# Kernel tuning notes

Measured on AMD Instinct MI355X. Metric: run time of the kernel, lower is better.

## Reference

```python
import jax, jax.numpy as jnp
import numpy as np

N = 100_000      # nodes
E = 1_600_000    # edges (avg degree 16)
D_IN, D_PROJ, D_HID = 128, 128, 64


def setup_inputs() -> dict:
    key = jax.random.key(0)
    ks = jax.random.split(key, 10)
    glorot = lambda k, i, o: jax.random.normal(k, (i, o), jnp.float32) * jnp.sqrt(2.0 / (i + o))
    x = jax.random.normal(ks[0], (N, D_IN), jnp.float32)
    edge_index = jax.random.randint(ks[1], (2, E), 0, N, dtype=jnp.int32)
    # encoder: GCN(input->proj), ReLU, GCN(proj->hidden)
    W1, b1 = glorot(ks[2], D_IN, D_PROJ), jnp.zeros((D_PROJ,), jnp.float32)
    W2, b2 = glorot(ks[3], D_PROJ, D_HID), jnp.zeros((D_HID,), jnp.float32)
    # contra_head: GCN(hidden->proj), ReLU, GCN(proj->input)
    W3, b3 = glorot(ks[4], D_HID, D_PROJ), jnp.zeros((D_PROJ,), jnp.float32)
    W4, b4 = glorot(ks[5], D_PROJ, D_IN), jnp.zeros((D_IN,), jnp.float32)
    return dict(x=x, W1=W1, b1=b1, W2=W2, b2=b2, W3=W3, b3=b3, W4=W4, b4=b4,
                edge_index=edge_index)


def gcn_layer(x, W, b, src, dst, deg, inv_sqrt_deg):
    """PyG GCNConv: out = D^{-1/2}(A+I)D^{-1/2} (x W) + b, unit edge weights."""
    h = x @ W                                   # [N, out]
    norm = inv_sqrt_deg[src] * inv_sqrt_deg[dst]  # [E]
    agg = jax.ops.segment_sum(h[src] * norm[:, None], dst, num_segments=x.shape[0])
    agg = agg + h * (1.0 / deg)[:, None]        # self-loop term: 1/deg_i
    return agg + b


def reference(x, W1, b1, W2, b2, W3, b3, W4, b4, edge_index):
    src, dst = edge_index[0], edge_index[1]
    # gcn_norm degrees (with self-loop, unit weights) — shared across layers
    deg = jax.ops.segment_sum(jnp.ones(src.shape[0], x.dtype), dst,
                              num_segments=x.shape[0]) + 1.0
    isd = jax.lax.rsqrt(deg)
    # encoder
    z = gcn_layer(x, W1, b1, src, dst, deg, isd)
    z = jax.nn.relu(z)
    z = gcn_layer(z, W2, b2, src, dst, deg, isd)
    # contra_head
    z = gcn_layer(z, W3, b3, src, dst, deg, isd)
    z = jax.nn.relu(z)
    z = gcn_layer(z, W4, b4, src, dst, deg, isd)
    return z
```

## Files before the change

### kernel.cpp

```cpp
#include <hip/hip_runtime.h>
#include <hip/hip_fp16.h>

typedef _Float16 f16x8 __attribute__((ext_vector_type(8)));
typedef float f32x4 __attribute__((ext_vector_type(4)));

#define CHUNK 2048
#define BSHIFT 9
#define CAP 12288


static __global__ void binpass_kernel(const int* __restrict__ src, const int* __restrict__ dst,
                                      int* __restrict__ bucket_cur, int2* __restrict__ pairs,
                                      int E, int NB) {
  __shared__ int lh[256], lbase[256], lcur[256];
  int t = threadIdx.x;
  lh[t] = 0;
  __syncthreads();
  int base = blockIdx.x * CHUNK;
  int end = min(base + CHUNK, E);
  for (int i = base + t; i < end; i += 256)
    atomicAdd(&lh[dst[i] >> BSHIFT], 1);
  __syncthreads();
  if (t < NB && lh[t]) lbase[t] = atomicAdd(&bucket_cur[t], lh[t]);
  lcur[t] = 0;
  __syncthreads();
  for (int i = base + t; i < end; i += 256) {
    int s = src[i], d = dst[i];
    int b = d >> BSHIFT;
    int p = lbase[b] + atomicAdd(&lcur[b], 1);
    if (p < CAP) pairs[(size_t)b * CAP + p] = make_int2(s, d);
  }
}

static __global__ void bedge_scan_kernel(const int* __restrict__ bucket_cur,
                                         int* __restrict__ bucket_base,
                                         int* __restrict__ row_ptr, int NB, int n, int E) {
  __shared__ int sh[256];
  int t = threadIdx.x;
  int v = (t < NB) ? bucket_cur[t] : 0;
  sh[t] = v;
  __syncthreads();
  for (int off = 1; off < 256; off <<= 1) {
    int x = (t >= off) ? sh[t - off] : 0;
    __syncthreads();
    sh[t] += x;
    __syncthreads();
  }
  if (t < NB) bucket_base[t] = sh[t] - v;
  if (t == 0) row_ptr[n] = E;
}

static __global__ void bucket_work_kernel(const int2* __restrict__ pairs,
                                          const int* __restrict__ bucket_cur,
                                          const int* __restrict__ bucket_base,
                                          float* __restrict__ isd, int* __restrict__ row_ptr,
                                          int* __restrict__ csr_src, int n) {
  __shared__ int lcnt[512];
  __shared__ int lcur[512];
  __shared__ int s2[256];
  int b = blockIdx.x;
  int t = threadIdx.x;
  int d0 = b << BSHIFT;
  int cnt = bucket_cur[b];
  int base = bucket_base[b];
  const int2* bp = pairs + (size_t)b * CAP;
  lcnt[t] = 0;
  lcnt[t + 256] = 0;
  __syncthreads();
  for (int i = t; i < cnt; i += 256)
    atomicAdd(&lcnt[bp[i].y - d0], 1);
  __syncthreads();
  int a0 = lcnt[2 * t], a1 = lcnt[2 * t + 1];
  s2[t] = a0 + a1;
  __syncthreads();
  for (int off = 1; off < 256; off <<= 1) {
    int x = (t >= off) ? s2[t - off] : 0;
    __syncthreads();
    s2[t] += x;
    __syncthreads();
  }
  int excl = s2[t] - (a0 + a1);
  int d = d0 + 2 * t;
  if (d < n)     { row_ptr[d]     = base + excl;      isd[d]     = rsqrtf((float)a0 + 1.0f); }
  if (d + 1 < n) { row_ptr[d + 1] = base + excl + a0; isd[d + 1] = rsqrtf((float)a1 + 1.0f); }
  lcur[2 * t] = excl;
  lcur[2 * t + 1] = excl + a0;
  __syncthreads();
  for (int i = t; i < cnt; i += 256) {
    int2 e = bp[i];
    int p = atomicAdd(&lcur[e.y - d0], 1);
    csr_src[base + p] = e.x;
  }
}

template<int K, int NOUT, bool AHALF, int EPI>
__device__ __forceinline__ void gemm_mfma_body(const void* __restrict__ Xin,
                                               const float* __restrict__ W,
                                               const float* __restrict__ aux,
                                               __half* __restrict__ H, int n) {
  __shared__ _Float16 ah[64][K + 8];
  __shared__ _Float16 bh[64][K + 8];
  const int tid = threadIdx.x;
  const int bm = blockIdx.x * 64;
  const int bc = blockIdx.y * 64;

  if (AHALF) {
    const __half* Xh = (const __half*)Xin;
    for (int i = tid; i < 64 * (K / 8); i += 256) {
      int r = i / (K / 8), c8 = i % (K / 8);
      int gr = bm + r;
      f16x8 v = {};
      if (gr < n) v = *(const f16x8*)&Xh[(size_t)gr * K + c8 * 8];
      *(f16x8*)&ah[r][c8 * 8] = v;
    }
  } else {
    const float* Xf = (const float*)Xin;
    for (int i = tid; i < 64 * (K / 8); i += 256) {
      int r = i / (K / 8), c8 = i % (K / 8);
      int gr = bm + r;
      f16x8 v = {};
      if (gr < n) {
        float4 a = *(const float4*)&Xf[(size_t)gr * K + c8 * 8];
        float4 b = *(const float4*)&Xf[(size_t)gr * K + c8 * 8 + 4];
        v[0] = (_Float16)a.x; v[1] = (_Float16)a.y; v[2] = (_Float16)a.z; v[3] = (_Float16)a.w;
        v[4] = (_Float16)b.x; v[5] = (_Float16)b.y; v[6] = (_Float16)b.z; v[7] = (_Float16)b.w;
      }
      *(f16x8*)&ah[r][c8 * 8] = v;
    }
  }
  {
    const int nn = tid & 63;
    const int kq = tid >> 6;
    constexpr int KT = K / 4;
#pragma unroll
    for (int k8 = 0; k8 < KT; k8 += 8) {
      int k0 = kq * KT + k8;
      f16x8 v;
#pragma unroll
      for (int j = 0; j < 8; ++j)
        v[j] = (_Float16)W[(size_t)(k0 + j) * NOUT + bc + nn];
      *(f16x8*)&bh[nn][k0] = v;
    }
  }
  __syncthreads();

  const int lane = tid & 63;
  const int wid = tid >> 6;
  const int wm = (wid >> 1) * 32;
  const int wn = (wid & 1) * 32;
  const int lr = lane & 15;
  const int lk = (lane >> 4) * 8;

  f32x4 acc[2][2] = {};
#pragma unroll
  for (int ks = 0; ks < K; ks += 32) {
    f16x8 a0 = *(const f16x8*)&ah[wm + lr][ks + lk];
    f16x8 a1 = *(const f16x8*)&ah[wm + 16 + lr][ks + lk];
    f16x8 b0 = *(const f16x8*)&bh[wn + lr][ks + lk];
    f16x8 b1 = *(const f16x8*)&bh[wn + 16 + lr][ks + lk];
    acc[0][0] = __builtin_amdgcn_mfma_f32_16x16x32_f16(a0, b0, acc[0][0], 0, 0, 0);
    acc[0][1] = __builtin_amdgcn_mfma_f32_16x16x32_f16(a0, b1, acc[0][1], 0, 0, 0);
    acc[1][0] = __builtin_amdgcn_mfma_f32_16x16x32_f16(a1, b0, acc[1][0], 0, 0, 0);
    acc[1][1] = __builtin_amdgcn_mfma_f32_16x16x32_f16(a1, b1, acc[1][1], 0, 0, 0);
  }

  float bcol0 = 0.f, bcol1 = 0.f;
  if (EPI == 1) {
    bcol0 = aux[bc + wn + lr];
    bcol1 = aux[bc + wn + 16 + lr];
  }
  const int rgrp = (lane >> 4) * 4;
#pragma unroll
  for (int tm = 0; tm < 2; ++tm) {
    int rb = bm + wm + tm * 16 + rgrp;
#pragma unroll
    for (int r = 0; r < 4; ++r) {
      int row = rb + r;
      if (row >= n) continue;
      float s = (EPI == 0) ? aux[row] : 0.f;
#pragma unroll
      for (int tn = 0; tn < 2; ++tn) {
        int col = bc + wn + tn * 16 + lr;
        float v = acc[tm][tn][r];
        if (EPI == 0) v *= s;
        else v = fmaxf(v + (tn ? bcol1 : bcol0), 0.f);
        H[(size_t)row * NOUT + col] = __float2half(v);
      }
    }
  }
}

#define DEF_GEMM(NAME, K, NOUT, AHALF, EPI)                                              \
  __global__ __launch_bounds__(256, 2) void NAME(const void* __restrict__ X,             \
                                                 const float* __restrict__ W,            \
                                                 const float* __restrict__ aux,          \
                                                 __half* __restrict__ H, int n) {        \
    gemm_mfma_body<K, NOUT, AHALF, EPI>(X, W, aux, H, n);                                \
  }
DEF_GEMM(gemm1_mfma_k128_n128, 128, 128, false, 0)
DEF_GEMM(gemm2_mfma_k128_n64, 128, 64, true, 0)
DEF_GEMM(gemm3_mfma_k64_n128, 64, 128, true, 1)
DEF_GEMM(gemm4_mfma_k128_n128, 128, 128, true, 0)

template<int D, bool RELU, bool HASBIAS, bool POSTSCALE, bool OUTHALF>
__device__ __forceinline__ void agg_body(const __half* __restrict__ hs, const int* __restrict__ row_ptr,
                                         const int* __restrict__ csr_src, const float* __restrict__ isd,
                                         const float* __restrict__ bias, void* __restrict__ out, int n) {
  int gt = blockIdx.x * blockDim.x + threadIdx.x;
  int gw, l;
  if (D == 128) {
    gw = gt >> 6;
    l = threadIdx.x & 63;
  } else {
    gw = (gt >> 6) * 2 + ((threadIdx.x >> 5) & 1);
    l = threadIdx.x & 31;
  }
  if (gw >= n) return;

  float wd = isd[gw];
  float2 hv = __half22float2(*(const __half2*)(hs + (size_t)gw * D + l * 2));
  float2 bv = make_float2(0.f, 0.f);
  if (HASBIAS) bv = *(const float2*)(bias + l * 2);

  int beg = row_ptr[gw], end = row_ptr[gw + 1];
  float acc0 = 0.f, acc1 = 0.f;

  int e = beg;
  int s0 = 0, s1 = 0, s2 = 0, s3 = 0;
  if (e + 4 <= end) {
    s0 = csr_src[e + 0]; s1 = csr_src[e + 1];
    s2 = csr_src[e + 2]; s3 = csr_src[e + 3];
  }
  while (e + 4 <= end) {
    float2 v0 = __half22float2(*(const __half2*)(hs + (size_t)s0 * D + l * 2));
    float2 v1 = __half22float2(*(const __half2*)(hs + (size_t)s1 * D + l * 2));
    float2 v2 = __half22float2(*(const __half2*)(hs + (size_t)s2 * D + l * 2));
    float2 v3 = __half22float2(*(const __half2*)(hs + (size_t)s3 * D + l * 2));
    int en = e + 4;
    if (en + 4 <= end) {
      s0 = csr_src[en + 0]; s1 = csr_src[en + 1];
      s2 = csr_src[en + 2]; s3 = csr_src[en + 3];
    }
    acc0 += (v0.x + v1.x) + (v2.x + v3.x);
    acc1 += (v0.y + v1.y) + (v2.y + v3.y);
    e = en;
  }
  for (; e < end; ++e) {
    int s = csr_src[e];
    float2 v = __half22float2(*(const __half2*)(hs + (size_t)s * D + l * 2));
    acc0 += v.x;
    acc1 += v.y;
  }

  float o0 = wd * (acc0 + hv.x);
  float o1 = wd * (acc1 + hv.y);
  if (HASBIAS) { o0 += bv.x; o1 += bv.y; }
  if (RELU) { o0 = fmaxf(o0, 0.f); o1 = fmaxf(o1, 0.f); }
  if (POSTSCALE) { o0 *= wd; o1 *= wd; }
  if (OUTHALF) {
    *(__half2*)((__half*)out + (size_t)gw * D + l * 2) = __floats2half2_rn(o0, o1);
  } else {
    *(float2*)((float*)out + (size_t)gw * D + l * 2) = make_float2(o0, o1);
  }
}

#define DEF_AGG(NAME, D, RELU, HASBIAS, POSTSCALE, OUTHALF)                                \
  __global__ void NAME(const __half* __restrict__ hs, const int* __restrict__ row_ptr,     \
                       const int* __restrict__ csr_src, const float* __restrict__ isd,     \
                       const float* __restrict__ bias, void* __restrict__ out, int n) {    \
    agg_body<D, RELU, HASBIAS, POSTSCALE, OUTHALF>(hs, row_ptr, csr_src, isd, bias, out, n); \
  }
DEF_AGG(agg1_d128_biasrelu_f16, 128, true, true, false, true)
DEF_AGG(agg2_d64_bias_ps_f16, 64, false, true, true, true)
DEF_AGG(agg3_d64_plain_f16, 64, false, false, false, true)
DEF_AGG(agg4_d128_bias_f32, 128, false, true, false, false)

static inline size_t align_up(size_t x, size_t a) { return (x + a - 1) & ~(a - 1); }

extern "C" void kernel_launch(void* const* d_in, const int* in_sizes, int n_in,
                              void* d_out, int out_size, void* d_ws, size_t ws_size,
                              hipStream_t stream) {
  const float* X  = (const float*)d_in[0];
  const float* W1 = (const float*)d_in[1];
  const float* b1 = (const float*)d_in[2];
  const float* W2 = (const float*)d_in[3];
  const float* b2 = (const float*)d_in[4];
  const float* W3 = (const float*)d_in[5];
  const float* b3 = (const float*)d_in[6];
  const float* W4 = (const float*)d_in[7];
  const float* b4 = (const float*)d_in[8];
  const int*   ei = (const int*)d_in[9];

  const int N = in_sizes[0] / 128;
  const int E = in_sizes[9] / 2;
  const int* src = ei;
  const int* dst = ei + E;
  float* OUT = (float*)d_out;

  const int NB = (N + (1 << BSHIFT) - 1) >> BSHIFT;
  const int NCH = (E + CHUNK - 1) / CHUNK;

  char* ws = (char*)d_ws;
  size_t off = 0;
  auto alloc = [&](size_t bytes) { void* p = ws + off; off = align_up(off + bytes, 256); return p; };
  int*    row_ptr     = (int*)alloc(((size_t)N + 1) * 4);
  float*  isd         = (float*)alloc((size_t)N * 4);
  int*    csr_src     = (int*)alloc((size_t)E * 4);
  int*    bucket_cur  = (int*)alloc(256 * 4);
  int*    bucket_base = (int*)alloc(256 * 4);
  __half* B1          = (__half*)alloc((size_t)N * 128 * 2);
  __half* B2          = (__half*)alloc((size_t)N * 128 * 2);
  __half* Fa = B1;
  __half* Fb = B1 + (size_t)N * 64;
  int2*   pairs = (int2*)B1;

  hipMemsetAsync(bucket_cur, 0, 256 * 4, stream);

  binpass_kernel<<<NCH, 256, 0, stream>>>(src, dst, bucket_cur, pairs, E, NB);
  bedge_scan_kernel<<<1, 256, 0, stream>>>(bucket_cur, bucket_base, row_ptr, NB, N, E);
  bucket_work_kernel<<<NB, 256, 0, stream>>>(pairs, bucket_cur, bucket_base, isd, row_ptr, csr_src, N);

  const int gm = (N + 63) / 64;
  const int ab128 = (int)(((size_t)N * 64 + 255) / 256);
  const int ab64  = (int)(((size_t)N * 32 + 255) / 256);

  gemm1_mfma_k128_n128<<<dim3(gm, 2), 256, 0, stream>>>(X, W1, isd, B1, N);
  agg1_d128_biasrelu_f16<<<ab128, 256, 0, stream>>>(B1, row_ptr, csr_src, isd, b1, B2, N);
  gemm2_mfma_k128_n64<<<dim3(gm, 1), 256, 0, stream>>>(B2, W2, isd, Fa, N);
  agg2_d64_bias_ps_f16<<<ab64, 256, 0, stream>>>(Fa, row_ptr, csr_src, isd, b2, Fb, N);
  agg3_d64_plain_f16<<<ab64, 256, 0, stream>>>(Fb, row_ptr, csr_src, isd, nullptr, Fa, N);
  gemm3_mfma_k64_n128<<<dim3(gm, 2), 256, 0, stream>>>(Fa, W3, b3, B2, N);
  gemm4_mfma_k128_n128<<<dim3(gm, 2), 256, 0, stream>>>(B2, W4, isd, B1, N);
  agg4_d128_bias_f32<<<ab128, 256, 0, stream>>>(B1, row_ptr, csr_src, isd, b4, OUT, N);
}
```

Baseline: 333.9 us.

## Pre-convert inputs and weights to fp16, widen GEMM tiles, vectorize aggregation lanes

Adds a separate kernel that converts X to fp16 and another that transposes all weights to fp16 once, so the GEMMs load pre-transposed half weights with vector loads. Each GEMM block now computes the full output width instead of splitting columns across two blocks, which avoids reloading the A tile. The aggregation kernels switch to 4 halves per lane, packing more nodes per wavefront. The binning chunk size is also doubled. The X conversion adds an extra pass over the input in exchange for cheaper GEMM loads.

```diff
diff --git a/kernel.cpp b/kernel.cpp
--- a/kernel.cpp
+++ b/kernel.cpp
@@ -2,9 +2,10 @@
 #include <hip/hip_fp16.h>
 
 typedef _Float16 f16x8 __attribute__((ext_vector_type(8)));
+typedef _Float16 f16x4 __attribute__((ext_vector_type(4)));
 typedef float f32x4 __attribute__((ext_vector_type(4)));
 
-#define CHUNK 2048
+#define CHUNK 4096
 #define BSHIFT 9
 #define CAP 12288
 
@@ -93,82 +94,84 @@
   }
 }
 
-template<int K, int NOUT, bool AHALF, int EPI>
-__device__ __forceinline__ void gemm_mfma_body(const void* __restrict__ Xin,
-                                               const float* __restrict__ W,
+static __global__ void cvt_x_kernel(const float* __restrict__ X, __half* __restrict__ Xh,
+                                    int total8) {
+  int i = blockIdx.x * blockDim.x + threadIdx.x;
+  if (i >= total8) return;
+  float4 a = *(const float4*)&X[(size_t)i * 8];
+  float4 b = *(const float4*)&X[(size_t)i * 8 + 4];
+  f16x8 v;
+  v[0] = (_Float16)a.x; v[1] = (_Float16)a.y; v[2] = (_Float16)a.z; v[3] = (_Float16)a.w;
+  v[4] = (_Float16)b.x; v[5] = (_Float16)b.y; v[6] = (_Float16)b.z; v[7] = (_Float16)b.w;
+  *(f16x8*)&Xh[(size_t)i * 8] = v;
+}
+
+static __global__ void wt_all_kernel(const float* __restrict__ W1, const float* __restrict__ W2,
+                                     const float* __restrict__ W3, const float* __restrict__ W4,
+                                     __half* __restrict__ T1, __half* __restrict__ T2,
+                                     __half* __restrict__ T3, __half* __restrict__ T4) {
+  int m = blockIdx.y;
+  const float* W; __half* T; int K, NO, sh;
+  if (m == 0)      { W = W1; T = T1; K = 128; NO = 128; sh = 7; }
+  else if (m == 1) { W = W2; T = T2; K = 128; NO = 64;  sh = 6; }
+  else if (m == 2) { W = W3; T = T3; K = 64;  NO = 128; sh = 7; }
+  else             { W = W4; T = T4; K = 128; NO = 128; sh = 7; }
+  int total = K * NO;
+  for (int idx = blockIdx.x * 256 + threadIdx.x; idx < total; idx += gridDim.x * 256) {
+    int k = idx >> sh, c = idx & (NO - 1);
+    T[(size_t)c * K + k] = __float2half(W[idx]);
+  }
+}
+
+template<int K, int NOUT, int EPI>
+__device__ __forceinline__ void gemm_mfma_body(const __half* __restrict__ Xh,
+                                               const __half* __restrict__ Wt,
                                                const float* __restrict__ aux,
                                                __half* __restrict__ H, int n) {
   __shared__ _Float16 ah[64][K + 8];
-  __shared__ _Float16 bh[64][K + 8];
+  __shared__ _Float16 bh[NOUT][K + 8];
   const int tid = threadIdx.x;
   const int bm = blockIdx.x * 64;
-  const int bc = blockIdx.y * 64;
-
-  if (AHALF) {
-    const __half* Xh = (const __half*)Xin;
-    for (int i = tid; i < 64 * (K / 8); i += 256) {
-      int r = i / (K / 8), c8 = i % (K / 8);
-      int gr = bm + r;
-      f16x8 v = {};
-      if (gr < n) v = *(const f16x8*)&Xh[(size_t)gr * K + c8 * 8];
-      *(f16x8*)&ah[r][c8 * 8] = v;
-    }
-  } else {
-    const float* Xf = (const float*)Xin;
-    for (int i = tid; i < 64 * (K / 8); i += 256) {
-      int r = i / (K / 8), c8 = i % (K / 8);
-      int gr = bm + r;
-      f16x8 v = {};
-      if (gr < n) {
-        float4 a = *(const float4*)&Xf[(size_t)gr * K + c8 * 8];
-        float4 b = *(const float4*)&Xf[(size_t)gr * K + c8 * 8 + 4];
-        v[0] = (_Float16)a.x; v[1] = (_Float16)a.y; v[2] = (_Float16)a.z; v[3] = (_Float16)a.w;
-        v[4] = (_Float16)b.x; v[5] = (_Float16)b.y; v[6] = (_Float16)b.z; v[7] = (_Float16)b.w;
-      }
-      *(f16x8*)&ah[r][c8 * 8] = v;
-    }
-  }
-  {
-    const int nn = tid & 63;
-    const int kq = tid >> 6;
-    constexpr int KT = K / 4;
-#pragma unroll
-    for (int k8 = 0; k8 < KT; k8 += 8) {
-      int k0 = kq * KT + k8;
-      f16x8 v;
-#pragma unroll
-      for (int j = 0; j < 8; ++j)
-        v[j] = (_Float16)W[(size_t)(k0 + j) * NOUT + bc + nn];
-      *(f16x8*)&bh[nn][k0] = v;
-    }
+
+  for (int i = tid; i < 64 * (K / 8); i += 256) {
+    int r = i / (K / 8), c8 = i % (K / 8);
+    int gr = bm + r;
+    f16x8 v = {};
+    if (gr < n) v = *(const f16x8*)&Xh[(size_t)gr * K + c8 * 8];
+    *(f16x8*)&ah[r][c8 * 8] = v;
+  }
+  for (int i = tid; i < NOUT * (K / 8); i += 256) {
+    int c = i / (K / 8), k8 = i % (K / 8);
+    *(f16x8*)&bh[c][k8 * 8] = *(const f16x8*)&Wt[(size_t)c * K + k8 * 8];
   }
   __syncthreads();
 
   const int lane = tid & 63;
   const int wid = tid >> 6;
+  constexpr int WN = NOUT / 2;
+  constexpr int NF = WN / 16;
   const int wm = (wid >> 1) * 32;
-  const int wn = (wid & 1) * 32;
+  const int wn = (wid & 1) * WN;
   const int lr = lane & 15;
   const int lk = (lane >> 4) * 8;
 
-  f32x4 acc[2][2] = {};
+  f32x4 acc[2][NF] = {};
 #pragma unroll
   for (int ks = 0; ks < K; ks += 32) {
     f16x8 a0 = *(const f16x8*)&ah[wm + lr][ks + lk];
     f16x8 a1 = *(const f16x8*)&ah[wm + 16 + lr][ks + lk];
-    f16x8 b0 = *(const f16x8*)&bh[wn + lr][ks + lk];
-    f16x8 b1 = *(const f16x8*)&bh[wn + 16 + lr][ks + lk];
-    acc[0][0] = __builtin_amdgcn_mfma_f32_16x16x32_f16(a0, b0, acc[0][0], 0, 0, 0);
-    acc[0][1] = __builtin_amdgcn_mfma_f32_16x16x32_f16(a0, b1, acc[0][1], 0, 0, 0);
-    acc[1][0] = __builtin_amdgcn_mfma_f32_16x16x32_f16(a1, b0, acc[1][0], 0, 0, 0);
-    acc[1][1] = __builtin_amdgcn_mfma_f32_16x16x32_f16(a1, b1, acc[1][1], 0, 0, 0);
-  }
-
-  float bcol0 = 0.f, bcol1 = 0.f;
-  if (EPI == 1) {
-    bcol0 = aux[bc + wn + lr];
-    bcol1 = aux[bc + wn + 16 + lr];
-  }
+#pragma unroll
+    for (int tn = 0; tn < NF; ++tn) {
+      f16x8 b = *(const f16x8*)&bh[wn + tn * 16 + lr][ks + lk];
+      acc[0][tn] = __builtin_amdgcn_mfma_f32_16x16x32_f16(a0, b, acc[0][tn], 0, 0, 0);
+      acc[1][tn] = __builtin_amdgcn_mfma_f32_16x16x32_f16(a1, b, acc[1][tn], 0, 0, 0);
+    }
+  }
+
+  float bcol[NF];
+#pragma unroll
+  for (int tn = 0; tn < NF; ++tn)
+    bcol[tn] = (EPI == 1) ? aux[wn + tn * 16 + lr] : 0.f;
   const int rgrp = (lane >> 4) * 4;
 #pragma unroll
   for (int tm = 0; tm < 2; ++tm) {
@@ -179,51 +182,46 @@
       if (row >= n) continue;
       float s = (EPI == 0) ? aux[row] : 0.f;
 #pragma unroll
-      for (int tn = 0; tn < 2; ++tn) {
-        int col = bc + wn + tn * 16 + lr;
+      for (int tn = 0; tn < NF; ++tn) {
         float v = acc[tm][tn][r];
         if (EPI == 0) v *= s;
-        else v = fmaxf(v + (tn ? bcol1 : bcol0), 0.f);
-        H[(size_t)row * NOUT + col] = __float2half(v);
+        else v = fmaxf(v + bcol[tn], 0.f);
+        H[(size_t)row * NOUT + wn + tn * 16 + lr] = __float2half(v);
       }
     }
   }
 }
 
-#define DEF_GEMM(NAME, K, NOUT, AHALF, EPI)                                              \
-  __global__ __launch_bounds__(256, 2) void NAME(const void* __restrict__ X,             \
-                                                 const float* __restrict__ W,            \
+#define DEF_GEMM(NAME, K, NOUT, EPI)                                                     \
+  __global__ __launch_bounds__(256, 2) void NAME(const __half* __restrict__ Xh,          \
+                                                 const __half* __restrict__ Wt,          \
                                                  const float* __restrict__ aux,          \
                                                  __half* __restrict__ H, int n) {        \
-    gemm_mfma_body<K, NOUT, AHALF, EPI>(X, W, aux, H, n);                                \
-  }
-DEF_GEMM(gemm1_mfma_k128_n128, 128, 128, false, 0)
-DEF_GEMM(gemm2_mfma_k128_n64, 128, 64, true, 0)
-DEF_GEMM(gemm3_mfma_k64_n128, 64, 128, true, 1)
-DEF_GEMM(gemm4_mfma_k128_n128, 128, 128, true, 0)
+    gemm_mfma_body<K, NOUT, EPI>(Xh, Wt, aux, H, n);                                     \
+  }
+DEF_GEMM(gemm1_mfma_k128_n128, 128, 128, 0)
+DEF_GEMM(gemm2_mfma_k128_n64, 128, 64, 0)
+DEF_GEMM(gemm3_mfma_k64_n128, 64, 128, 1)
+DEF_GEMM(gemm4_mfma_k128_n128, 128, 128, 0)
 
 template<int D, bool RELU, bool HASBIAS, bool POSTSCALE, bool OUTHALF>
 __device__ __forceinline__ void agg_body(const __half* __restrict__ hs, const int* __restrict__ row_ptr,
                                          const int* __restrict__ csr_src, const float* __restrict__ isd,
                                          const float* __restrict__ bias, void* __restrict__ out, int n) {
-  int gt = blockIdx.x * blockDim.x + threadIdx.x;
-  int gw, l;
-  if (D == 128) {
-    gw = gt >> 6;
-    l = threadIdx.x & 63;
-  } else {
-    gw = (gt >> 6) * 2 + ((threadIdx.x >> 5) & 1);
-    l = threadIdx.x & 31;
-  }
+  constexpr int LPN = D / 4;
+  int w = (blockIdx.x * blockDim.x + threadIdx.x) >> 6;
+  int lane = threadIdx.x & 63;
+  int li = lane & (LPN - 1);
+  int gw = w * (64 / LPN) + (lane / LPN);
   if (gw >= n) return;
 
   float wd = isd[gw];
-  float2 hv = __half22float2(*(const __half2*)(hs + (size_t)gw * D + l * 2));
-  float2 bv = make_float2(0.f, 0.f);
-  if (HASBIAS) bv = *(const float2*)(bias + l * 2);
+  f16x4 hv = *(const f16x4*)(hs + (size_t)gw * D + li * 4);
+  float4 bv = make_float4(0.f, 0.f, 0.f, 0.f);
+  if (HASBIAS) bv = *(const float4*)(bias + li * 4);
 
   int beg = row_ptr[gw], end = row_ptr[gw + 1];
-  float acc0 = 0.f, acc1 = 0.f;
+  float a0 = 0.f, a1 = 0.f, a2 = 0.f, a3 = 0.f;
 
   int e = beg;
   int s0 = 0, s1 = 0, s2 = 0, s3 = 0;
@@ -232,35 +230,43 @@
     s2 = csr_src[e + 2]; s3 = csr_src[e + 3];
   }
   while (e + 4 <= end) {
-    float2 v0 = __half22float2(*(const __half2*)(hs + (size_t)s0 * D + l * 2));
-    float2 v1 = __half22float2(*(const __half2*)(hs + (size_t)s1 * D + l * 2));
-    float2 v2 = __half22float2(*(const __half2*)(hs + (size_t)s2 * D + l * 2));
-    float2 v3 = __half22float2(*(const __half2*)(hs + (size_t)s3 * D + l * 2));
+    f16x4 v0 = *(const f16x4*)(hs + (size_t)s0 * D + li * 4);
+    f16x4 v1 = *(const f16x4*)(hs + (size_t)s1 * D + li * 4);
+    f16x4 v2 = *(const f16x4*)(hs + (size_t)s2 * D + li * 4);
+    f16x4 v3 = *(const f16x4*)(hs + (size_t)s3 * D + li * 4);
     int en = e + 4;
     if (en + 4 <= end) {
       s0 = csr_src[en + 0]; s1 = csr_src[en + 1];
       s2 = csr_src[en + 2]; s3 = csr_src[en + 3];
     }
-    acc0 += (v0.x + v1.x) + (v2.x + v3.x);
-    acc1 += (v0.y + v1.y) + (v2.y + v3.y);
+    a0 += ((float)v0[0] + (float)v1[0]) + ((float)v2[0] + (float)v3[0]);
+    a1 += ((float)v0[1] + (float)v1[1]) + ((float)v2[1] + (float)v3[1]);
+    a2 += ((float)v0[2] + (float)v1[2]) + ((float)v2[2] + (float)v3[2]);
+    a3 += ((float)v0[3] + (float)v1[3]) + ((float)v2[3] + (float)v3[3]);
     e = en;
   }
   for (; e < end; ++e) {
     int s = csr_src[e];
-    float2 v = __half22float2(*(const __half2*)(hs + (size_t)s * D + l * 2));
-    acc0 += v.x;
-    acc1 += v.y;
-  }
-
-  float o0 = wd * (acc0 + hv.x);
-  float o1 = wd * (acc1 + hv.y);
-  if (HASBIAS) { o0 += bv.x; o1 += bv.y; }
-  if (RELU) { o0 = fmaxf(o0, 0.f); o1 = fmaxf(o1, 0.f); }
-  if (POSTSCALE) { o0 *= wd; o1 *= wd; }
+    f16x4 v = *(const f16x4*)(hs + (size_t)s * D + li * 4);
+    a0 += (float)v[0]; a1 += (float)v[1]; a2 += (float)v[2]; a3 += (float)v[3];
+  }
+
+  float o0 = wd * (a0 + (float)hv[0]);
+  float o1 = wd * (a1 + (float)hv[1]);
+  float o2 = wd * (a2 + (float)hv[2]);
+  float o3 = wd * (a3 + (float)hv[3]);
+  if (HASBIAS) { o0 += bv.x; o1 += bv.y; o2 += bv.z; o3 += bv.w; }
+  if (RELU) {
+    o0 = fmaxf(o0, 0.f); o1 = fmaxf(o1, 0.f);
+    o2 = fmaxf(o2, 0.f); o3 = fmaxf(o3, 0.f);
+  }
+  if (POSTSCALE) { o0 *= wd; o1 *= wd; o2 *= wd; o3 *= wd; }
   if (OUTHALF) {
-    *(__half2*)((__half*)out + (size_t)gw * D + l * 2) = __floats2half2_rn(o0, o1);
+    f16x4 ov;
+    ov[0] = (_Float16)o0; ov[1] = (_Float16)o1; ov[2] = (_Float16)o2; ov[3] = (_Float16)o3;
+    *(f16x4*)((__half*)out + (size_t)gw * D + li * 4) = ov;
   } else {
-    *(float2*)((float*)out + (size_t)gw * D + l * 2) = make_float2(o0, o1);
+    *(float4*)((float*)out + (size_t)gw * D + li * 4) = make_float4(o0, o1, o2, o3);
   }
 }
 
@@ -308,8 +314,13 @@
   int*    csr_src     = (int*)alloc((size_t)E * 4);
   int*    bucket_cur  = (int*)alloc(256 * 4);
   int*    bucket_base = (int*)alloc(256 * 4);
+  __half* Wt1         = (__half*)alloc(128 * 128 * 2);
+  __half* Wt2         = (__half*)alloc(128 * 64 * 2);
+  __half* Wt3         = (__half*)alloc(64 * 128 * 2);
+  __half* Wt4         = (__half*)alloc(128 * 128 * 2);
+  __half* Xh          = (__half*)alloc((size_t)N * 128 * 2);
   __half* B1          = (__half*)alloc((size_t)N * 128 * 2);
-  __half* B2          = (__half*)alloc((size_t)N * 128 * 2);
+  __half* B2 = Xh;
   __half* Fa = B1;
   __half* Fb = B1 + (size_t)N * 64;
   int2*   pairs = (int2*)B1;
@@ -320,16 +331,20 @@
   bedge_scan_kernel<<<1, 256, 0, stream>>>(bucket_cur, bucket_base, row_ptr, NB, N, E);
   bucket_work_kernel<<<NB, 256, 0, stream>>>(pairs, bucket_cur, bucket_base, isd, row_ptr, csr_src, N);
 
+  int total8 = N * 128 / 8;
+  cvt_x_kernel<<<(total8 + 255) / 256, 256, 0, stream>>>(X, Xh, total8);
+  wt_all_kernel<<<dim3(16, 4), 256, 0, stream>>>(W1, W2, W3, W4, Wt1, Wt2, Wt3, Wt4);
+
   const int gm = (N + 63) / 64;
-  const int ab128 = (int)(((size_t)N * 64 + 255) / 256);
-  const int ab64  = (int)(((size_t)N * 32 + 255) / 256);
-
-  gemm1_mfma_k128_n128<<<dim3(gm, 2), 256, 0, stream>>>(X, W1, isd, B1, N);
+  const int ab128 = (N + 7) / 8;
+  const int ab64  = (N + 15) / 16;
+
+  gemm1_mfma_k128_n128<<<gm, 256, 0, stream>>>(Xh, Wt1, isd, B1, N);
   agg1_d128_biasrelu_f16<<<ab128, 256, 0, stream>>>(B1, row_ptr, csr_src, isd, b1, B2, N);
-  gemm2_mfma_k128_n64<<<dim3(gm, 1), 256, 0, stream>>>(B2, W2, isd, Fa, N);
+  gemm2_mfma_k128_n64<<<gm, 256, 0, stream>>>(B2, Wt2, isd, Fa, N);
   agg2_d64_bias_ps_f16<<<ab64, 256, 0, stream>>>(Fa, row_ptr, csr_src, isd, b2, Fb, N);
   agg3_d64_plain_f16<<<ab64, 256, 0, stream>>>(Fb, row_ptr, csr_src, isd, nullptr, Fa, N);
-  gemm3_mfma_k64_n128<<<dim3(gm, 2), 256, 0, stream>>>(Fa, W3, b3, B2, N);
-  gemm4_mfma_k128_n128<<<dim3(gm, 2), 256, 0, stream>>>(B2, W4, isd, B1, N);
+  gemm3_mfma_k64_n128<<<gm, 256, 0, stream>>>(Fa, Wt3, b3, B2, N);
+  gemm4_mfma_k128_n128<<<gm, 256, 0, stream>>>(B2, Wt4, isd, B1, N);
   agg4_d128_bias_f32<<<ab128, 256, 0, stream>>>(B1, row_ptr, csr_src, isd, b4, OUT, N);
 }
```

After: 318.0 us. 1.05x faster.
